# Optimization experiments

Measured on AMD Instinct MI355X. Metric: run time of the kernel, lower is better.

The kernel has to match this reference:

```python
import jax, jax.numpy as jnp
import numpy as np

B, S, F = 512, 512, 128   # batch, seq_len, facts_size (= querry_size)
H1, H2 = 80, 40
PAD = float(-2**32 + 1)


def setup_inputs() -> dict:
    key = jax.random.key(0)
    ks = jax.random.split(key, 12)
    inp = {
        "query": jax.random.normal(ks[0], (B, F), jnp.float32),
        "facts": jax.random.normal(ks[1], (B, S, F), jnp.float32),
        "mask": jax.random.randint(ks[2], (B, S), 0, 2, jnp.int32),
        # mlp1: querry_size -> facts_size
        "W1": jax.random.normal(ks[3], (F, F), jnp.float32) / np.sqrt(F),
        "b1": jnp.zeros((F,), jnp.float32),
        # PReLU alpha (per-feature, init zeros)
        "alpha": jnp.zeros((F,), jnp.float32),
        # mlp2: 4*F -> 80
        "W2": jax.random.normal(ks[4], (4 * F, H1), jnp.float32) / np.sqrt(4 * F),
        "b2": jnp.zeros((H1,), jnp.float32),
        # mlp3: 80 -> 40
        "W3": jax.random.normal(ks[5], (H1, H2), jnp.float32) / np.sqrt(H1),
        "b3": jnp.zeros((H2,), jnp.float32),
        # mlp4: 40 -> 1
        "W4": jax.random.normal(ks[6], (H2, 1), jnp.float32) / np.sqrt(H2),
        "b4": jnp.zeros((1,), jnp.float32),
    }
    return inp


def reference(query, facts, mask, W1, b1, alpha, W2, b2, W3, b3, W4, b4):
    # mlp1 + PReLU on the query
    q = query @ W1 + b1                                   # [B, F]
    q = jnp.where(q >= 0, q, alpha * q)                   # PReLU, alpha per-feature
    # broadcast query over sequence (tile+reshape in the original)
    qs = jnp.broadcast_to(q[:, None, :], (q.shape[0], S, F))  # [B, S, F]
    din = jnp.concatenate([qs, facts, qs - facts, qs * facts], axis=-1)  # [B,S,4F]
    h1 = jax.nn.sigmoid(din @ W2 + b2)                    # [B, S, 80]
    h2 = jax.nn.sigmoid(h1 @ W3 + b3)                     # [B, S, 40]
    scores = (h2 @ W4 + b4)[..., 0][:, None, :]           # [B, 1, S]
    key_masks = (mask == 1)[:, None, :]                   # [B, 1, S]
    scores = jnp.where(key_masks, scores, PAD)
    scores = jax.nn.softmax(scores, axis=-1)              # softmax over seq
    out = jnp.einsum("bqs,bsf->bqf", scores, facts)       # [B, 1, F]  (mode SUM)
    return out
```

## Files before the change

kernel.cpp:

```cpp
#include <hip/hip_runtime.h>
#include <hip/hip_bf16.h>

typedef __bf16 bf16x8 __attribute__((ext_vector_type(8)));
typedef float  f32x4  __attribute__((ext_vector_type(4)));

#define WBT_STRIDE 136
#define H1_STRIDE  104
#define W3T_STRIDE 104

__global__ __launch_bounds__(512, 4)
void attn_fcn_kernel(const float* __restrict__ query,
                     const float* __restrict__ facts,
                     const int*   __restrict__ mask,
                     const float* __restrict__ W1,
                     const float* __restrict__ b1,
                     const float* __restrict__ alpha,
                     const float* __restrict__ W2,
                     const float* __restrict__ b2,
                     const float* __restrict__ W3,
                     const float* __restrict__ b3,
                     const float* __restrict__ W4,
                     const float* __restrict__ b4,
                     float* __restrict__ out)
{
    __shared__ float  qy[128];
    __shared__ float  qs[128];
    __shared__ float  qconst[80];
    __shared__ float  w4s[48];
    __shared__ float  b3s[48];
    __shared__ __align__(16) __bf16 WbT[80 * WBT_STRIDE];
    __shared__ __align__(16) __bf16 W3T[48 * W3T_STRIDE];
    __shared__ __align__(16) __bf16 h1sB[8][16 * H1_STRIDE];
    __shared__ float  scores[512];
    __shared__ float  wred[8];
    __shared__ float  wsum[8];
    __shared__ float  outacc[4][128];

    const int b = blockIdx.x;
    const int t = threadIdx.x;

    if (t < 128) qy[t] = query[b * 128 + t];
    for (int e = t; e < 48 * W3T_STRIDE; e += 512) W3T[e] = (__bf16)0.0f;
    for (int e = t; e < 8 * 16 * H1_STRIDE; e += 512) (&h1sB[0][0])[e] = (__bf16)0.0f;
    if (t < 48) {
        w4s[t] = (t < 40) ? W4[t] : 0.0f;
        b3s[t] = (t < 40) ? b3[t] : 0.0f;
    }
    __syncthreads();

    for (int e = t; e < 80 * 40; e += 512) {
        int k = e / 40, j = e % 40;
        W3T[j * W3T_STRIDE + k] = (__bf16)W3[e];
    }
    if (t < 128) {
        float acc = b1[t];
        #pragma unroll 4
        for (int k = 0; k < 128; ++k) acc = fmaf(qy[k], W1[k * 128 + t], acc);
        float a = alpha[t];
        qs[t] = (acc >= 0.0f) ? acc : a * acc;
    }
    __syncthreads();

    if (t < 80) {
        float acc = b2[t];
        #pragma unroll 4
        for (int k = 0; k < 128; ++k)
            acc = fmaf(qs[k], W2[k * 80 + t] + W2[(256 + k) * 80 + t], acc);
        qconst[t] = acc;
    }
    for (int e = t; e < 128 * 80; e += 512) {
        int k = e / 80, n = e % 80;
        float w = W2[(128 + k) * 80 + n] - W2[(256 + k) * 80 + n]
                + qs[k] * W2[(384 + k) * 80 + n];
        WbT[n * WBT_STRIDE + k] = (__bf16)w;
    }
    __syncthreads();

    const int wave = t >> 6;
    const int lane = t & 63;
    const int qd   = lane >> 4;
    const int m    = lane & 15;
    const float* fb = facts + (size_t)b * (512 * 128);
    const int*   mb = mask + b * 512;
    __bf16* h1w = &h1sB[wave][0];
    const int wbase = wave * 64;

    f32x4 av[4][2];
    {
        const float* p0 = &fb[(size_t)(wbase + m) * 128 + qd * 8];
        #pragma unroll
        for (int kc = 0; kc < 4; ++kc) {
            av[kc][0] = *(const f32x4*)(p0 + kc * 32);
            av[kc][1] = *(const f32x4*)(p0 + kc * 32 + 4);
        }
    }

    for (int tile = 0; tile < 4; ++tile) {
        const int s0 = wbase + tile * 16;

        bf16x8 af[4];
        #pragma unroll
        for (int kc = 0; kc < 4; ++kc)
            #pragma unroll
            for (int i = 0; i < 8; ++i)
                af[kc][i] = (__bf16)((i < 4) ? av[kc][0][i] : av[kc][1][i - 4]);

        if (tile < 3) {
            const float* pn = &fb[(size_t)(s0 + 16 + m) * 128 + qd * 8];
            #pragma unroll
            for (int kc = 0; kc < 4; ++kc) {
                av[kc][0] = *(const f32x4*)(pn + kc * 32);
                av[kc][1] = *(const f32x4*)(pn + kc * 32 + 4);
            }
        }

        #pragma unroll
        for (int ct = 0; ct < 5; ++ct) {
            f32x4 acc = {0.f, 0.f, 0.f, 0.f};
            #pragma unroll
            for (int kc = 0; kc < 4; ++kc) {
                bf16x8 bfr = *(const bf16x8*)&WbT[(ct * 16 + m) * WBT_STRIDE + kc * 32 + qd * 8];
                acc = __builtin_amdgcn_mfma_f32_16x16x32_bf16(af[kc], bfr, acc, 0, 0, 0);
            }
            const int col = ct * 16 + m;
            const float qc = qconst[col];
            #pragma unroll
            for (int r = 0; r < 4; ++r) {
                float x = acc[r] + qc;
                float h = __builtin_amdgcn_rcpf(1.0f + __expf(-x));
                h1w[(qd * 4 + r) * H1_STRIDE + col] = (__bf16)h;
            }
        }
        asm volatile("s_waitcnt lgkmcnt(0)" ::: "memory");

        bf16x8 a2[3];
        #pragma unroll
        for (int kc = 0; kc < 3; ++kc)
            a2[kc] = *(const bf16x8*)&h1w[m * H1_STRIDE + kc * 32 + qd * 8];
        float sc[4] = {0.f, 0.f, 0.f, 0.f};
        #pragma unroll
        for (int ct = 0; ct < 3; ++ct) {
            f32x4 acc2 = {0.f, 0.f, 0.f, 0.f};
            #pragma unroll
            for (int kc = 0; kc < 3; ++kc) {
                bf16x8 bfr = *(const bf16x8*)&W3T[(ct * 16 + m) * W3T_STRIDE + kc * 32 + qd * 8];
                acc2 = __builtin_amdgcn_mfma_f32_16x16x32_bf16(a2[kc], bfr, acc2, 0, 0, 0);
            }
            const int col = ct * 16 + m;
            const float w4v = w4s[col], b3v = b3s[col];
            #pragma unroll
            for (int r = 0; r < 4; ++r) {
                float h2 = __builtin_amdgcn_rcpf(1.0f + __expf(-(acc2[r] + b3v)));
                sc[r] = fmaf(h2, w4v, sc[r]);
            }
        }
        #pragma unroll
        for (int d = 1; d < 16; d <<= 1)
            #pragma unroll
            for (int r = 0; r < 4; ++r)
                sc[r] += __shfl_xor(sc[r], d);
        if (m == 0) {
            #pragma unroll
            for (int r = 0; r < 4; ++r)
                scores[s0 + qd * 4 + r] = sc[r];
        }
    }
    __syncthreads();

    const float b4v = b4[0];
    float v = scores[t] + b4v;
    if (mb[t] != 1) v = -INFINITY;
    float r = v;
    #pragma unroll
    for (int d = 1; d < 64; d <<= 1) r = fmaxf(r, __shfl_xor(r, d));
    if (lane == 0) wred[wave] = r;
    __syncthreads();
    float gmax = wred[0];
    #pragma unroll
    for (int w = 1; w < 8; ++w) gmax = fmaxf(gmax, wred[w]);
    float e = (gmax == -INFINITY) ? 1.0f : __expf(v - gmax);
    float z = e;
    #pragma unroll
    for (int d = 1; d < 64; d <<= 1) z += __shfl_xor(z, d);
    if (lane == 0) wsum[wave] = z;
    scores[t] = e;
    __syncthreads();
    float Zg = wsum[0];
    #pragma unroll
    for (int w = 1; w < 8; ++w) Zg += wsum[w];

    {
        const int f   = t & 127;
        const int qtr = t >> 7;
        const float* fp = fb + (size_t)qtr * 128 * 128 + f;
        const float* pp = &scores[qtr * 128];
        float a0 = 0.f, a1 = 0.f, a2 = 0.f, a3 = 0.f;
        #pragma unroll 4
        for (int s = 0; s < 128; s += 4) {
            a0 = fmaf(pp[s],     fp[(size_t)(s)     * 128], a0);
            a1 = fmaf(pp[s + 1], fp[(size_t)(s + 1) * 128], a1);
            a2 = fmaf(pp[s + 2], fp[(size_t)(s + 2) * 128], a2);
            a3 = fmaf(pp[s + 3], fp[(size_t)(s + 3) * 128], a3);
        }
        outacc[qtr][f] = (a0 + a1) + (a2 + a3);
    }
    __syncthreads();
    if (t < 128)
        out[b * 128 + t] =
            ((outacc[0][t] + outacc[1][t]) + (outacc[2][t] + outacc[3][t])) / Zg;
}

extern "C" void kernel_launch(void* const* d_in, const int* in_sizes, int n_in,
                              void* d_out, int out_size, void* d_ws, size_t ws_size,
                              hipStream_t stream) {
    (void)in_sizes; (void)n_in; (void)d_ws; (void)ws_size; (void)out_size;
    const float* query = (const float*)d_in[0];
    const float* facts = (const float*)d_in[1];
    const int*   mask  = (const int*)d_in[2];
    const float* W1 = (const float*)d_in[3];
    const float* b1 = (const float*)d_in[4];
    const float* al = (const float*)d_in[5];
    const float* W2 = (const float*)d_in[6];
    const float* b2 = (const float*)d_in[7];
    const float* W3 = (const float*)d_in[8];
    const float* b3 = (const float*)d_in[9];
    const float* W4 = (const float*)d_in[10];
    const float* b4 = (const float*)d_in[11];
    attn_fcn_kernel<<<dim3(512), dim3(512), 0, stream>>>(
        query, facts, mask, W1, b1, al, W2, b2, W3, b3, W4, b4, (float*)d_out);
}
```

Baseline: 256.7 us.

## Fuse softmax and weighted facts sum into the MLP tile loop

Each wave now exponentiates its own masked scores and accumulates the probability-weighted facts rows it already holds in registers. This removes the separate scores buffer, the two block-wide max/sum reductions and the second pass that re-read all of facts from memory. The query-side matvecs (W1, and the qconst part of W2) are split across 4x more threads with partial sums. The tile loop no longer prefetches the next tile. The softmax drops the max subtraction and b4, which is exact in theory because the sigmoid-bounded scores cannot overflow exp. An all-masked row would now give 0/0 where the reference gives a uniform average.

```diff
diff --git a/kernel.cpp b/kernel.cpp
--- a/kernel.cpp
+++ b/kernel.cpp
@@ -9,110 +9,104 @@
 #define W3T_STRIDE 104
 
 __global__ __launch_bounds__(512, 4)
-void attn_fcn_kernel(const float* __restrict__ query,
-                     const float* __restrict__ facts,
-                     const int*   __restrict__ mask,
-                     const float* __restrict__ W1,
-                     const float* __restrict__ b1,
-                     const float* __restrict__ alpha,
-                     const float* __restrict__ W2,
-                     const float* __restrict__ b2,
-                     const float* __restrict__ W3,
-                     const float* __restrict__ b3,
-                     const float* __restrict__ W4,
-                     const float* __restrict__ b4,
-                     float* __restrict__ out)
+void attn_fused(const float* __restrict__ query,
+                const float* __restrict__ facts,
+                const int*   __restrict__ mask,
+                const float* __restrict__ W1, const float* __restrict__ b1,
+                const float* __restrict__ alpha,
+                const float* __restrict__ W2, const float* __restrict__ b2,
+                const float* __restrict__ W3, const float* __restrict__ b3,
+                const float* __restrict__ W4,
+                float* __restrict__ out)
 {
-    __shared__ float  qy[128];
-    __shared__ float  qs[128];
-    __shared__ float  qconst[80];
-    __shared__ float  w4s[48];
-    __shared__ float  b3s[48];
     __shared__ __align__(16) __bf16 WbT[80 * WBT_STRIDE];
     __shared__ __align__(16) __bf16 W3T[48 * W3T_STRIDE];
-    __shared__ __align__(16) __bf16 h1sB[8][16 * H1_STRIDE];
-    __shared__ float  scores[512];
-    __shared__ float  wred[8];
-    __shared__ float  wsum[8];
-    __shared__ float  outacc[4][128];
-
-    const int b = blockIdx.x;
-    const int t = threadIdx.x;
+    __shared__ __align__(16) __bf16 h1all[128 * H1_STRIDE];
+    __shared__ float qy[128], qs[128], qcs[80];
+    __shared__ float qpart[4][128], qcp[4][80];
+    __shared__ float w4s[48], b3s[48];
+    __shared__ float outw[8 * 128];
+    __shared__ float Zw[8];
+
+    const int b = blockIdx.x, t = threadIdx.x;
 
     if (t < 128) qy[t] = query[b * 128 + t];
-    for (int e = t; e < 48 * W3T_STRIDE; e += 512) W3T[e] = (__bf16)0.0f;
-    for (int e = t; e < 8 * 16 * H1_STRIDE; e += 512) (&h1sB[0][0])[e] = (__bf16)0.0f;
-    if (t < 48) {
-        w4s[t] = (t < 40) ? W4[t] : 0.0f;
-        b3s[t] = (t < 40) ? b3[t] : 0.0f;
-    }
-    __syncthreads();
-
-    for (int e = t; e < 80 * 40; e += 512) {
-        int k = e / 40, j = e % 40;
-        W3T[j * W3T_STRIDE + k] = (__bf16)W3[e];
-    }
+    for (int e = t; e < 48 * 96; e += 512) {
+        int j = e / 96, k = e % 96;
+        W3T[j * W3T_STRIDE + k] = (j < 40 && k < 80) ? (__bf16)W3[k * 40 + j]
+                                                     : (__bf16)0.0f;
+    }
+    for (int e = t; e < 128 * 16; e += 512) {
+        int r = e >> 4, c = 80 + (e & 15);
+        h1all[r * H1_STRIDE + c] = (__bf16)0.0f;
+    }
+    if (t < 48) { w4s[t] = (t < 40) ? W4[t] : 0.f; b3s[t] = (t < 40) ? b3[t] : 0.f; }
+    __syncthreads();
+
+    {
+        int j = t & 127, kh = t >> 7;
+        float acc = (kh == 0) ? b1[j] : 0.f;
+        const float* w1p = W1 + (kh * 32) * 128 + j;
+        #pragma unroll 8
+        for (int k = 0; k < 32; ++k) acc = fmaf(qy[kh * 32 + k], w1p[k * 128], acc);
+        qpart[kh][j] = acc;
+    }
+    __syncthreads();
     if (t < 128) {
-        float acc = b1[t];
-        #pragma unroll 4
-        for (int k = 0; k < 128; ++k) acc = fmaf(qy[k], W1[k * 128 + t], acc);
-        float a = alpha[t];
-        qs[t] = (acc >= 0.0f) ? acc : a * acc;
-    }
-    __syncthreads();
-
-    if (t < 80) {
-        float acc = b2[t];
-        #pragma unroll 4
-        for (int k = 0; k < 128; ++k)
-            acc = fmaf(qs[k], W2[k * 80 + t] + W2[(256 + k) * 80 + t], acc);
-        qconst[t] = acc;
+        float s = (qpart[0][t] + qpart[1][t]) + (qpart[2][t] + qpart[3][t]);
+        qs[t] = (s >= 0.f) ? s : alpha[t] * s;
+    }
+    __syncthreads();
+
+    if (t < 320) {
+        int jj = t % 80, hh = t / 80;
+        float acc = (hh == 0) ? b2[jj] : 0.f;
+        #pragma unroll 8
+        for (int k = hh * 32; k < hh * 32 + 32; ++k)
+            acc = fmaf(qs[k], W2[k * 80 + jj] + W2[(256 + k) * 80 + jj], acc);
+        qcp[hh][jj] = acc;
     }
     for (int e = t; e < 128 * 80; e += 512) {
-        int k = e / 80, n = e % 80;
+        int k = e / 80, n = e - k * 80;
         float w = W2[(128 + k) * 80 + n] - W2[(256 + k) * 80 + n]
                 + qs[k] * W2[(384 + k) * 80 + n];
         WbT[n * WBT_STRIDE + k] = (__bf16)w;
     }
     __syncthreads();
-
-    const int wave = t >> 6;
-    const int lane = t & 63;
-    const int qd   = lane >> 4;
-    const int m    = lane & 15;
+    if (t < 80) qcs[t] = (qcp[0][t] + qcp[1][t]) + (qcp[2][t] + qcp[3][t]);
+    __syncthreads();
+
+    const int wave = t >> 6, lane = t & 63, qd = lane >> 4, m = lane & 15;
     const float* fb = facts + (size_t)b * (512 * 128);
     const int*   mb = mask + b * 512;
-    __bf16* h1w = &h1sB[wave][0];
-    const int wbase = wave * 64;
-
-    f32x4 av[4][2];
-    {
-        const float* p0 = &fb[(size_t)(wbase + m) * 128 + qd * 8];
-        #pragma unroll
-        for (int kc = 0; kc < 4; ++kc) {
-            av[kc][0] = *(const f32x4*)(p0 + kc * 32);
-            av[kc][1] = *(const f32x4*)(p0 + kc * 32 + 4);
+    __bf16* h1w = &h1all[wave * 16 * H1_STRIDE];
+
+    float oacc[4][8];
+    #pragma unroll
+    for (int kc = 0; kc < 4; ++kc)
+        #pragma unroll
+        for (int i = 0; i < 8; ++i) oacc[kc][i] = 0.f;
+    float Zl = 0.f;
+
+    for (int tile = 0; tile < 4; ++tile) {
+        const int s0 = wave * 64 + tile * 16;
+        const int mv = mb[s0 + m];
+
+        f32x4 av[4][2];
+        {
+            const float* p0 = &fb[(size_t)(s0 + m) * 128 + qd * 8];
+            #pragma unroll
+            for (int kc = 0; kc < 4; ++kc) {
+                av[kc][0] = *(const f32x4*)(p0 + kc * 32);
+                av[kc][1] = *(const f32x4*)(p0 + kc * 32 + 4);
+            }
         }
-    }
-
-    for (int tile = 0; tile < 4; ++tile) {
-        const int s0 = wbase + tile * 16;
-
         bf16x8 af[4];
         #pragma unroll
         for (int kc = 0; kc < 4; ++kc)
             #pragma unroll
             for (int i = 0; i < 8; ++i)
                 af[kc][i] = (__bf16)((i < 4) ? av[kc][0][i] : av[kc][1][i - 4]);
-
-        if (tile < 3) {
-            const float* pn = &fb[(size_t)(s0 + 16 + m) * 128 + qd * 8];
-            #pragma unroll
-            for (int kc = 0; kc < 4; ++kc) {
-                av[kc][0] = *(const f32x4*)(pn + kc * 32);
-                av[kc][1] = *(const f32x4*)(pn + kc * 32 + 4);
-            }
-        }
 
         #pragma unroll
         for (int ct = 0; ct < 5; ++ct) {
@@ -123,7 +117,7 @@
                 acc = __builtin_amdgcn_mfma_f32_16x16x32_bf16(af[kc], bfr, acc, 0, 0, 0);
             }
             const int col = ct * 16 + m;
-            const float qc = qconst[col];
+            const float qc = qcs[col];
             #pragma unroll
             for (int r = 0; r < 4; ++r) {
                 float x = acc[r] + qc;
@@ -159,55 +153,51 @@
             #pragma unroll
             for (int r = 0; r < 4; ++r)
                 sc[r] += __shfl_xor(sc[r], d);
-        if (m == 0) {
-            #pragma unroll
-            for (int r = 0; r < 4; ++r)
-                scores[s0 + qd * 4 + r] = sc[r];
-        }
-    }
-    __syncthreads();
-
-    const float b4v = b4[0];
-    float v = scores[t] + b4v;
-    if (mb[t] != 1) v = -INFINITY;
-    float r = v;
+
+        const int idx = ((((m >> 2) << 4) | m) << 2);
+        float s0v = __int_as_float(__builtin_amdgcn_ds_bpermute(idx, __float_as_int(sc[0])));
+        float s1v = __int_as_float(__builtin_amdgcn_ds_bpermute(idx, __float_as_int(sc[1])));
+        float s2v = __int_as_float(__builtin_amdgcn_ds_bpermute(idx, __float_as_int(sc[2])));
+        float s3v = __int_as_float(__builtin_amdgcn_ds_bpermute(idx, __float_as_int(sc[3])));
+        const int rr = m & 3;
+        float srow = (rr == 0) ? s0v : (rr == 1) ? s1v : (rr == 2) ? s2v : s3v;
+
+        const float pm = (mv == 1) ? __expf(srow) : 0.f;
+        Zl += pm;
+        #pragma unroll
+        for (int kc = 0; kc < 4; ++kc)
+            #pragma unroll
+            for (int i = 0; i < 4; ++i) {
+                oacc[kc][i]     = fmaf(pm, av[kc][0][i], oacc[kc][i]);
+                oacc[kc][i + 4] = fmaf(pm, av[kc][1][i], oacc[kc][i + 4]);
+            }
+    }
+
     #pragma unroll
-    for (int d = 1; d < 64; d <<= 1) r = fmaxf(r, __shfl_xor(r, d));
-    if (lane == 0) wred[wave] = r;
-    __syncthreads();
-    float gmax = wred[0];
-    #pragma unroll
-    for (int w = 1; w < 8; ++w) gmax = fmaxf(gmax, wred[w]);
-    float e = (gmax == -INFINITY) ? 1.0f : __expf(v - gmax);
-    float z = e;
-    #pragma unroll
-    for (int d = 1; d < 64; d <<= 1) z += __shfl_xor(z, d);
-    if (lane == 0) wsum[wave] = z;
-    scores[t] = e;
-    __syncthreads();
-    float Zg = wsum[0];
-    #pragma unroll
-    for (int w = 1; w < 8; ++w) Zg += wsum[w];
-
-    {
-        const int f   = t & 127;
-        const int qtr = t >> 7;
-        const float* fp = fb + (size_t)qtr * 128 * 128 + f;
-        const float* pp = &scores[qtr * 128];
-        float a0 = 0.f, a1 = 0.f, a2 = 0.f, a3 = 0.f;
-        #pragma unroll 4
-        for (int s = 0; s < 128; s += 4) {
-            a0 = fmaf(pp[s],     fp[(size_t)(s)     * 128], a0);
-            a1 = fmaf(pp[s + 1], fp[(size_t)(s + 1) * 128], a1);
-            a2 = fmaf(pp[s + 2], fp[(size_t)(s + 2) * 128], a2);
-            a3 = fmaf(pp[s + 3], fp[(size_t)(s + 3) * 128], a3);
-        }
-        outacc[qtr][f] = (a0 + a1) + (a2 + a3);
-    }
-    __syncthreads();
-    if (t < 128)
-        out[b * 128 + t] =
-            ((outacc[0][t] + outacc[1][t]) + (outacc[2][t] + outacc[3][t])) / Zg;
+    for (int d = 1; d < 16; d <<= 1) {
+        #pragma unroll
+        for (int kc = 0; kc < 4; ++kc)
+            #pragma unroll
+            for (int i = 0; i < 8; ++i)
+                oacc[kc][i] += __shfl_xor(oacc[kc][i], d);
+        Zl += __shfl_xor(Zl, d);
+    }
+    if (m == 0) {
+        #pragma unroll
+        for (int kc = 0; kc < 4; ++kc)
+            #pragma unroll
+            for (int i = 0; i < 8; ++i)
+                outw[wave * 128 + kc * 32 + qd * 8 + i] = oacc[kc][i];
+        if (lane == 0) Zw[wave] = Zl;
+    }
+    __syncthreads();
+
+    if (t < 128) {
+        float v = 0.f, Z = 0.f;
+        #pragma unroll
+        for (int w = 0; w < 8; ++w) { v += outw[w * 128 + t]; Z += Zw[w]; }
+        out[b * 128 + t] = v / Z;
+    }
 }
 
 extern "C" void kernel_launch(void* const* d_in, const int* in_sizes, int n_in,
@@ -226,6 +216,7 @@
     const float* b3 = (const float*)d_in[9];
     const float* W4 = (const float*)d_in[10];
     const float* b4 = (const float*)d_in[11];
-    attn_fcn_kernel<<<dim3(512), dim3(512), 0, stream>>>(
-        query, facts, mask, W1, b1, al, W2, b2, W3, b3, W4, b4, (float*)d_out);
+    (void)b4;
+    attn_fused<<<dim3(512), dim3(512), 0, stream>>>(
+        query, facts, mask, W1, b1, al, W2, b2, W3, b3, W4, (float*)d_out);
 }
```

Measured after the change: 233.2 us. 9.2% less time.
